# Optimization experiments

Hardware: AMD Instinct MI355X
Metric: run time of the kernel (lower is better)

The kernel has to match this reference:

```python
import jax, jax.numpy as jnp
import numpy as np

N_NODES = 100000
N_EDGES = 1600000
IN_DIM = 64
OUT_DIM = 64


def setup_inputs() -> dict:
    key = jax.random.key(0)
    k1, k2, k3, k4, k5, k6 = jax.random.split(key, 6)
    # xavier-uniform-ish scales for the linear weights (gain=1.414)
    fc_bound = 1.414 * np.sqrt(6.0 / (IN_DIM + OUT_DIM))
    at_bound = 1.414 * np.sqrt(6.0 / (OUT_DIM + 1))
    return {
        "h_src": jax.random.normal(k1, (N_NODES, IN_DIM), dtype=jnp.float32),
        "h_dst": jax.random.normal(k2, (N_NODES, IN_DIM), dtype=jnp.float32),
        "W_fc": jax.random.uniform(k3, (OUT_DIM, IN_DIM), dtype=jnp.float32,
                                   minval=-fc_bound, maxval=fc_bound),
        "w_attn": jax.random.uniform(k4, (OUT_DIM,), dtype=jnp.float32,
                                     minval=-at_bound, maxval=at_bound),
        "src": jax.random.randint(k5, (N_EDGES,), 0, N_NODES, dtype=jnp.int64),
        "dst": jnp.sort(jax.random.randint(k6, (N_EDGES,), 0, N_NODES, dtype=jnp.int64)),
    }


def reference(h_src, h_dst, W_fc, w_attn, src, dst):
    # Per-edge feature difference: dst - src  (edge_attention)
    diff_e = h_dst[dst] - h_src[src]                      # [E, in_dim]
    # fc projection (dropout p=0 in eval) then attention score
    d = diff_e @ W_fc.T                                   # [E, out_dim]
    e = jnp.tanh(d @ w_attn)                              # [E]
    # Segment softmax over incoming edges of each destination node
    m = jax.ops.segment_max(e, dst, num_segments=N_NODES)  # [N], -inf for empty
    ex = jnp.exp(e - m[dst])                              # [E]
    s = jax.ops.segment_sum(ex, dst, num_segments=N_NODES)  # [N]
    alpha = ex / s[dst]                                   # [E]
    # Weighted sum aggregation of projected diffs per destination node
    h_diff = jax.ops.segment_sum(alpha[:, None] * d, dst, num_segments=N_NODES)  # [N, out_dim]
    return jax.nn.elu(h_diff)
```

## Files before the change

### kernel.cpp

```cpp
#include <hip/hip_runtime.h>
#include <hip/hip_fp16.h>
#include <math.h>

#define NN 100000
#define NE 1600000
#define DIM 64
#define HST 72
#define PROJ_BLOCKS ((2 * NN) / 64)
#define ROWPTR_BLOCKS ((NE + 255) / 256)

typedef __attribute__((ext_vector_type(8))) __fp16 half8;
typedef __attribute__((ext_vector_type(4))) float f32x4;

__device__ __forceinline__ __half2 u2h2(unsigned u) { __half2 h; __builtin_memcpy(&h, &u, 4); return h; }
__device__ __forceinline__ unsigned h22u(__half2 h) { unsigned u; __builtin_memcpy(&u, &h, 4); return u; }
__device__ __forceinline__ unsigned pk_f16(float a, float b) {
    auto h = __builtin_amdgcn_cvt_pkrtz(a, b);
    unsigned u; __builtin_memcpy(&u, &h, 4); return u;
}

__global__ __launch_bounds__(256) void proj_kernel(
    const float* __restrict__ h_src, const float* __restrict__ h_dst,
    const float* __restrict__ W, const float* __restrict__ w_attn,
    const int* __restrict__ dst, int* __restrict__ row_ptr,
    unsigned* __restrict__ p16, float* __restrict__ a_src, float* __restrict__ a_dst) {
    __shared__ __align__(16) unsigned short Hh[64 * HST];
    __shared__ __align__(16) unsigned short Wh[64 * HST];
    __shared__ float was[DIM];

    const int t = threadIdx.x;

    if (blockIdx.x >= PROJ_BLOCKS) {
        int i = (blockIdx.x - PROJ_BLOCKS) * 256 + t;
        if (i >= NE) return;
        int d = dst[i];
        int prev = (i == 0) ? -1 : dst[i - 1];
        for (int n = prev + 1; n <= d; ++n) row_ptr[n] = i;
        if (i == NE - 1) {
            for (int n = d + 1; n <= NN; ++n) row_ptr[n] = NE;
        }
        return;
    }

    const int row0 = blockIdx.x * 64;

#pragma unroll
    for (int r = 0; r < 4; ++r) {
        int idx = (r * 256 + t) * 4;
        int j = idx >> 6, k = idx & 63;
        float4 v = *(const float4*)(W + idx);
        uint2 pk; pk.x = pk_f16(v.x, v.y); pk.y = pk_f16(v.z, v.w);
        *(uint2*)((char*)Wh + j * (HST * 2) + k * 2) = pk;
    }
    if (t < DIM) was[t] = w_attn[t];

#pragma unroll
    for (int r = 0; r < 4; ++r) {
        int idx = (r * 256 + t) * 4;
        int row = idx >> 6, k = idx & 63;
        int grow = row0 + row;
        const float* hp = (grow < NN) ? h_src + (size_t)grow * DIM
                                      : h_dst + (size_t)(grow - NN) * DIM;
        float4 v = *(const float4*)(hp + k);
        uint2 pk; pk.x = pk_f16(v.x, v.y); pk.y = pk_f16(v.z, v.w);
        *(uint2*)((char*)Hh + row * (HST * 2) + k * 2) = pk;
    }
    __syncthreads();

    const int wv = t >> 6, lane = t & 63;
    const int col = lane & 15, quad = lane >> 4;
    const int m0 = wv * 16;

    const char* Hb = (const char*)Hh + (m0 + col) * (HST * 2) + quad * 16;
    half8 af0 = *(const half8*)(Hb);
    half8 af1 = *(const half8*)(Hb + 64);

    f32x4 c[4];
#pragma unroll
    for (int n = 0; n < 4; ++n) {
        const char* Bb = (const char*)Wh + (n * 16 + col) * (HST * 2) + quad * 16;
        half8 b0 = *(const half8*)(Bb);
        half8 b1 = *(const half8*)(Bb + 64);
        f32x4 acc = {0.f, 0.f, 0.f, 0.f};
        acc = __builtin_amdgcn_mfma_f32_16x16x32_f16(af0, b0, acc, 0, 0, 0);
        acc = __builtin_amdgcn_mfma_f32_16x16x32_f16(af1, b1, acc, 0, 0, 0);
        c[n] = acc;
    }

    float wv4[4];
#pragma unroll
    for (int n = 0; n < 4; ++n) wv4[n] = was[n * 16 + col];
#pragma unroll
    for (int reg = 0; reg < 4; ++reg) {
        float pa = c[0][reg] * wv4[0] + c[1][reg] * wv4[1] +
                   c[2][reg] * wv4[2] + c[3][reg] * wv4[3];
#pragma unroll
        for (int off = 1; off <= 8; off <<= 1) pa += __shfl_xor(pa, off);
        if (col == 0) {
            int grow = row0 + m0 + quad * 4 + reg;
            if (grow < NN) a_src[grow] = pa;
            else a_dst[grow - NN] = pa;
        }
    }

    __syncthreads();
    unsigned* Pd = (unsigned*)Hh;
#pragma unroll
    for (int n = 0; n < 4; ++n) {
#pragma unroll
        for (int reg = 0; reg < 4; ++reg) {
            float other = __shfl_xor(c[n][reg], 1);
            if (!(col & 1)) {
                unsigned pk = pk_f16(c[n][reg], other);
                Pd[(m0 + quad * 4 + reg) * 32 + (n * 16 + col) / 2] = pk;
            }
        }
    }
    __syncthreads();
#pragma unroll
    for (int r = 0; r < 2; ++r) {
        int idx = (r * 256 + t) * 4;
        uint4 v = *(const uint4*)(Pd + idx);
        *(uint4*)(p16 + (size_t)row0 * 32 + idx) = v;
    }
}

__global__ __launch_bounds__(256) void agg_kernel(
    const char* __restrict__ p16base,
    const float* __restrict__ a_src, const float* __restrict__ a_dst,
    const int* __restrict__ src, const int* __restrict__ row_ptr,
    float4* __restrict__ out4) {
    __shared__ uint2 buf[4][64];
    const int wv = threadIdx.x >> 6;
    const int lane = threadIdx.x & 63;
    const int g = lane >> 4;
    const int glane = lane & 15;
    const int sub16 = glane >> 3;
    const int chunk = glane & 7;

    const int wid = (blockIdx.x * 4 + wv) * 4 + g;
    if (wid >= NN) return;

    const int beg = row_ptr[wid];
    const int end = row_ptr[wid + 1];
    const bool nonempty = end > beg;

    if (!nonempty) {
        if (sub16 == 0) {
            const size_t ob = (size_t)wid * 16 + chunk * 2;
            out4[ob]     = make_float4(0.f, 0.f, 0.f, 0.f);
            out4[ob + 1] = make_float4(0.f, 0.f, 0.f, 0.f);
        }
        return;
    }

    const uint4 pdu = *(const uint4*)(p16base + ((size_t)(NN + wid)) * 128 + (size_t)chunk * 16);

    const float ad = a_dst[wid];
    const char* pbase = p16base + (size_t)chunk * 16;
    uint2* bufw = buf[wv];
    const int gbase = g * 16;

    float sAcc = 0.f;
    __half2 acc[4];
#pragma unroll
    for (int q = 0; q < 4; ++q) acc[q] = u2h2(0u);

    for (int cb = beg; cb < end; cb += 16) {
        int cd = end - cb; if (cd > 16) cd = 16;
        uint2 pk = make_uint2(0u, 0u);
        float w = 0.f;
        if (glane < cd) {
            int sv = src[cb + glane];
            float x = ad - a_src[sv];
            float th = 1.f - 2.f / (__expf(2.f * x) + 1.f);
            w = __expf(th);
            pk.x = pk_f16(w, w);
            pk.y = (unsigned)sv * 128u;
        }
        sAcc += w;
        bufw[lane] = pk;

        if (cd == 16) {
            uint2 e[8];
#pragma unroll
            for (int q = 0; q < 8; ++q) e[q] = bufw[gbase + 2 * q + sub16];
            uint4 r[8];
#pragma unroll
            for (int q = 0; q < 8; ++q) r[q] = *(const uint4*)(pbase + e[q].y);
#pragma unroll
            for (int q = 0; q < 8; ++q) {
                __half2 wq = u2h2(e[q].x);
                acc[0] = __hfma2(wq, u2h2(r[q].x), acc[0]);
                acc[1] = __hfma2(wq, u2h2(r[q].y), acc[1]);
                acc[2] = __hfma2(wq, u2h2(r[q].z), acc[2]);
                acc[3] = __hfma2(wq, u2h2(r[q].w), acc[3]);
            }
        } else {
            for (int j = 0; j < cd; j += 4) {
                uint2 e0 = bufw[gbase + j + sub16];
                uint2 e1 = bufw[gbase + j + 2 + sub16];
                uint4 r0 = *(const uint4*)(pbase + e0.y);
                uint4 r1 = *(const uint4*)(pbase + e1.y);
                __half2 w0 = u2h2(e0.x), w1 = u2h2(e1.x);
                acc[0] = __hfma2(w0, u2h2(r0.x), acc[0]);
                acc[1] = __hfma2(w0, u2h2(r0.y), acc[1]);
                acc[2] = __hfma2(w0, u2h2(r0.z), acc[2]);
                acc[3] = __hfma2(w0, u2h2(r0.w), acc[3]);
                acc[0] = __hfma2(w1, u2h2(r1.x), acc[0]);
                acc[1] = __hfma2(w1, u2h2(r1.y), acc[1]);
                acc[2] = __hfma2(w1, u2h2(r1.z), acc[2]);
                acc[3] = __hfma2(w1, u2h2(r1.w), acc[3]);
            }
        }
    }

#pragma unroll
    for (int off = 1; off <= 8; off <<= 1) sAcc += __shfl_xor(sAcc, off);
#pragma unroll
    for (int q = 0; q < 4; ++q)
        acc[q] = __hadd2(acc[q], u2h2(__shfl_xor(h22u(acc[q]), 8)));

    if (sub16 == 0) {
        const unsigned pw[4] = {pdu.x, pdu.y, pdu.z, pdu.w};
        const float inv = 1.f / sAcc;
        float o[8];
#pragma unroll
        for (int q = 0; q < 4; ++q) {
            float2 pf = __half22float2(u2h2(pw[q]));
            float2 af = __half22float2(acc[q]);
            float h0 = pf.x - af.x * inv;
            float h1 = pf.y - af.y * inv;
            o[2 * q]     = h0 > 0.f ? h0 : __expf(h0) - 1.f;
            o[2 * q + 1] = h1 > 0.f ? h1 : __expf(h1) - 1.f;
        }
        const size_t ob = (size_t)wid * 16 + chunk * 2;
        out4[ob]     = make_float4(o[0], o[1], o[2], o[3]);
        out4[ob + 1] = make_float4(o[4], o[5], o[6], o[7]);
    }
}

extern "C" void kernel_launch(void* const* d_in, const int* in_sizes, int n_in,
                              void* d_out, int out_size, void* d_ws, size_t ws_size,
                              hipStream_t stream) {
    const float* h_src = (const float*)d_in[0];
    const float* h_dst = (const float*)d_in[1];
    const float* W     = (const float*)d_in[2];
    const float* w_at  = (const float*)d_in[3];
    const int*   src   = (const int*)d_in[4];
    const int*   dst   = (const int*)d_in[5];

    char* ws = (char*)d_ws;
    unsigned* p16 = (unsigned*)ws;
    float* a_src = (float*)(ws + (size_t)2 * NN * 32 * 4);
    float* a_dst = a_src + NN;
    int* row_ptr = (int*)(a_dst + NN);

    hipLaunchKernelGGL(proj_kernel, dim3(PROJ_BLOCKS + ROWPTR_BLOCKS), dim3(256), 0, stream,
                       h_src, h_dst, W, w_at, dst, row_ptr, p16, a_src, a_dst);
    hipLaunchKernelGGL(agg_kernel, dim3((NN + 15) / 16), dim3(256), 0, stream,
                       (const char*)p16, a_src, a_dst, src, row_ptr,
                       (float4*)d_out);
}
```

Before: 150.6 us.

## Precompute per-edge weights and offsets in a separate edge kernel before aggregation

Adds an edge_kernel that computes each edge's softmax numerator (exp of tanh score) and the source row byte offset, packed as uint2 into a workspace array. The aggregation kernel then reads these packed pairs directly, dropping its LDS staging buffer, the per-chunk score computation and the partial-chunk branch. The goal is to shorten the dependent chain in the gather loop and make it more uniform. In exchange it adds a kernel launch and a 12.8 MB write and read of edge data. The denominator is now summed from fp16-rounded weights.

```diff
diff --git a/kernel.cpp b/kernel.cpp
--- a/kernel.cpp
+++ b/kernel.cpp
@@ -125,12 +125,35 @@
     }
 }
 
+__global__ __launch_bounds__(256) void edge_kernel(
+    const int* __restrict__ src, const int* __restrict__ dst,
+    const float* __restrict__ a_src, const float* __restrict__ a_dst,
+    uint2* __restrict__ ew) {
+    const int e0 = (blockIdx.x * 256 + threadIdx.x) * 4;
+    if (e0 >= NE) return;
+    int4 sv = *(const int4*)(src + e0);
+    int4 dv = *(const int4*)(dst + e0);
+    const int s[4] = {sv.x, sv.y, sv.z, sv.w};
+    const int d[4] = {dv.x, dv.y, dv.z, dv.w};
+    uint2 r[4];
+#pragma unroll
+    for (int j = 0; j < 4; ++j) {
+        float x = a_dst[d[j]] - a_src[s[j]];
+        float th = 1.f - 2.f / (__expf(2.f * x) + 1.f);
+        float w = __expf(th);
+        r[j].x = pk_f16(w, w);
+        r[j].y = (unsigned)s[j] * 128u;
+    }
+    uint4* o = (uint4*)(ew + e0);
+    o[0] = make_uint4(r[0].x, r[0].y, r[1].x, r[1].y);
+    o[1] = make_uint4(r[2].x, r[2].y, r[3].x, r[3].y);
+}
+
 __global__ __launch_bounds__(256) void agg_kernel(
     const char* __restrict__ p16base,
-    const float* __restrict__ a_src, const float* __restrict__ a_dst,
-    const int* __restrict__ src, const int* __restrict__ row_ptr,
+    const uint2* __restrict__ ew,
+    const int* __restrict__ row_ptr,
     float4* __restrict__ out4) {
-    __shared__ uint2 buf[4][64];
     const int wv = threadIdx.x >> 6;
     const int lane = threadIdx.x & 63;
     const int g = lane >> 4;
@@ -143,9 +166,8 @@
 
     const int beg = row_ptr[wid];
     const int end = row_ptr[wid + 1];
-    const bool nonempty = end > beg;
-
-    if (!nonempty) {
+
+    if (end <= beg) {
         if (sub16 == 0) {
             const size_t ob = (size_t)wid * 16 + chunk * 2;
             out4[ob]     = make_float4(0.f, 0.f, 0.f, 0.f);
@@ -156,10 +178,7 @@
 
     const uint4 pdu = *(const uint4*)(p16base + ((size_t)(NN + wid)) * 128 + (size_t)chunk * 16);
 
-    const float ad = a_dst[wid];
     const char* pbase = p16base + (size_t)chunk * 16;
-    uint2* bufw = buf[wv];
-    const int gbase = g * 16;
 
     float sAcc = 0.f;
     __half2 acc[4];
@@ -167,56 +186,30 @@
     for (int q = 0; q < 4; ++q) acc[q] = u2h2(0u);
 
     for (int cb = beg; cb < end; cb += 16) {
-        int cd = end - cb; if (cd > 16) cd = 16;
-        uint2 pk = make_uint2(0u, 0u);
-        float w = 0.f;
-        if (glane < cd) {
-            int sv = src[cb + glane];
-            float x = ad - a_src[sv];
-            float th = 1.f - 2.f / (__expf(2.f * x) + 1.f);
-            w = __expf(th);
-            pk.x = pk_f16(w, w);
-            pk.y = (unsigned)sv * 128u;
-        }
-        sAcc += w;
-        bufw[lane] = pk;
-
-        if (cd == 16) {
-            uint2 e[8];
-#pragma unroll
-            for (int q = 0; q < 8; ++q) e[q] = bufw[gbase + 2 * q + sub16];
-            uint4 r[8];
-#pragma unroll
-            for (int q = 0; q < 8; ++q) r[q] = *(const uint4*)(pbase + e[q].y);
-#pragma unroll
-            for (int q = 0; q < 8; ++q) {
-                __half2 wq = u2h2(e[q].x);
-                acc[0] = __hfma2(wq, u2h2(r[q].x), acc[0]);
-                acc[1] = __hfma2(wq, u2h2(r[q].y), acc[1]);
-                acc[2] = __hfma2(wq, u2h2(r[q].z), acc[2]);
-                acc[3] = __hfma2(wq, u2h2(r[q].w), acc[3]);
-            }
-        } else {
-            for (int j = 0; j < cd; j += 4) {
-                uint2 e0 = bufw[gbase + j + sub16];
-                uint2 e1 = bufw[gbase + j + 2 + sub16];
-                uint4 r0 = *(const uint4*)(pbase + e0.y);
-                uint4 r1 = *(const uint4*)(pbase + e1.y);
-                __half2 w0 = u2h2(e0.x), w1 = u2h2(e1.x);
-                acc[0] = __hfma2(w0, u2h2(r0.x), acc[0]);
-                acc[1] = __hfma2(w0, u2h2(r0.y), acc[1]);
-                acc[2] = __hfma2(w0, u2h2(r0.z), acc[2]);
-                acc[3] = __hfma2(w0, u2h2(r0.w), acc[3]);
-                acc[0] = __hfma2(w1, u2h2(r1.x), acc[0]);
-                acc[1] = __hfma2(w1, u2h2(r1.y), acc[1]);
-                acc[2] = __hfma2(w1, u2h2(r1.z), acc[2]);
-                acc[3] = __hfma2(w1, u2h2(r1.w), acc[3]);
-            }
-        }
-    }
-
-#pragma unroll
-    for (int off = 1; off <= 8; off <<= 1) sAcc += __shfl_xor(sAcc, off);
+        uint2 e[8];
+#pragma unroll
+        for (int q = 0; q < 8; ++q) {
+            int idx = cb + 2 * q + sub16;
+            uint2 v = make_uint2(0u, 0u);
+            if (idx < end) v = ew[idx];
+            e[q] = v;
+        }
+        uint4 r[8];
+#pragma unroll
+        for (int q = 0; q < 8; ++q) r[q] = *(const uint4*)(pbase + e[q].y);
+#pragma unroll
+        for (int q = 0; q < 8; ++q) {
+            __half2 wq = u2h2(e[q].x);
+            __half wl; __builtin_memcpy(&wl, &e[q].x, 2);
+            sAcc += __half2float(wl);
+            acc[0] = __hfma2(wq, u2h2(r[q].x), acc[0]);
+            acc[1] = __hfma2(wq, u2h2(r[q].y), acc[1]);
+            acc[2] = __hfma2(wq, u2h2(r[q].z), acc[2]);
+            acc[3] = __hfma2(wq, u2h2(r[q].w), acc[3]);
+        }
+    }
+
+    sAcc += __shfl_xor(sAcc, 8);
 #pragma unroll
     for (int q = 0; q < 4; ++q)
         acc[q] = __hadd2(acc[q], u2h2(__shfl_xor(h22u(acc[q]), 8)));
@@ -255,10 +248,14 @@
     float* a_src = (float*)(ws + (size_t)2 * NN * 32 * 4);
     float* a_dst = a_src + NN;
     int* row_ptr = (int*)(a_dst + NN);
+    size_t ew_off = (size_t)2 * NN * 32 * 4 + (size_t)2 * NN * 4 + (size_t)(NN + 1) * 4;
+    ew_off = (ew_off + 15) & ~(size_t)15;
+    uint2* ew = (uint2*)(ws + ew_off);
 
     hipLaunchKernelGGL(proj_kernel, dim3(PROJ_BLOCKS + ROWPTR_BLOCKS), dim3(256), 0, stream,
                        h_src, h_dst, W, w_at, dst, row_ptr, p16, a_src, a_dst);
+    hipLaunchKernelGGL(edge_kernel, dim3((NE / 4 + 255) / 256), dim3(256), 0, stream,
+                       src, dst, a_src, a_dst, ew);
     hipLaunchKernelGGL(agg_kernel, dim3((NN + 15) / 16), dim3(256), 0, stream,
-                       (const char*)p16, a_src, a_dst, src, row_ptr,
-                       (float4*)d_out);
-}
+                       (const char*)p16, ew, row_ptr, (float4*)d_out);
+}
```

After: 165.8 us. 1.1x slower.
